# Kernel optimization log

Hardware: AMD Instinct MI355X
Metric: run time of the kernel (lower is better)

## Reference

```python
import jax, jax.numpy as jnp
import numpy as np

N_USERS = 100000
N_ITEMS = 50000
N_NODES = N_USERS + N_ITEMS
N_EDGES = 3000000
EMBED_DIM = 64
N_LAYERS = 3


def setup_inputs() -> dict:
    key = jax.random.key(0)
    k1, k2, k3, k4, k5 = jax.random.split(key, 5)
    user_emb = 0.1 * jax.random.normal(k1, (N_USERS, EMBED_DIM), dtype=jnp.float32)
    item_emb = 0.1 * jax.random.normal(k2, (N_ITEMS, EMBED_DIM), dtype=jnp.float32)
    adj_rows = jax.random.randint(k3, (N_EDGES,), 0, N_NODES, dtype=jnp.int32)
    adj_cols = jax.random.randint(k4, (N_EDGES,), 0, N_NODES, dtype=jnp.int32)
    # mimic symmetric normalization scale (~1/avg_degree) so repeated SpMM stays stable
    avg_degree = N_EDGES / N_NODES
    adj_vals = jax.random.uniform(k5, (N_EDGES,), dtype=jnp.float32) / jnp.float32(avg_degree)
    return {"user_emb": user_emb, "item_emb": item_emb,
            "adj_rows": adj_rows, "adj_cols": adj_cols, "adj_vals": adj_vals}


def _spmm(rows, cols, vals, x):
    # y[r] = sum_{e: rows[e]==r} vals[e] * x[cols[e]]   (COO SpMM)
    msgs = vals[:, None] * x[cols]          # [E, d] gathered messages
    return jax.ops.segment_sum(msgs, rows, num_segments=N_NODES)


def reference(user_emb, item_emb, adj_rows, adj_cols, adj_vals):
    all_emb = jnp.concatenate([user_emb, item_emb], axis=0)  # [N, d]
    acc = all_emb
    cur = all_emb
    for _ in range(N_LAYERS):
        cur = _spmm(adj_rows, adj_cols, adj_vals, cur)
        acc = acc + cur
    final_emb = acc / jnp.float32(N_LAYERS + 1)  # mean over stacked layers
    return final_emb[:N_USERS], final_emb[N_USERS:]
```

## Files before the change

### kernel.cpp

```cpp
#include <hip/hip_runtime.h>
#include <cstddef>
#include <cstdint>

#define N_USERS 100000
#define N_ITEMS 50000
#define N_NODES 150000
#define N_EDGES 3000000

#define NBKT 586
#define BCHUNK 8192
#define ABLK ((N_EDGES + BCHUNK - 1) / BCHUNK)
#define NCLS 16
#define SCHUNK 3

#define VMAX  0.05f
#define QSCALE (16384.0f / VMAX)
#define DEQ    (VMAX / 16384.0f)

typedef unsigned int uint32;
typedef unsigned short ushort16;

__device__ __forceinline__ ushort16 f2b(float f) {
    uint32 b = __float_as_uint(f);
    b += 0x7FFFu + ((b >> 16) & 1u);
    return (ushort16)(b >> 16);
}
__device__ __forceinline__ float b2f(ushort16 h) {
    return __uint_as_float(((uint32)h) << 16);
}

#define CVT_BLOCKS ((N_NODES * 16 + 255) / 256)

__global__ __launch_bounds__(256) void k_cvt_count(const float* __restrict__ user,
                                                   const float* __restrict__ item,
                                                   ushort16* __restrict__ allb,
                                                   const int* __restrict__ rows,
                                                   int* __restrict__ bucket_cnt) {
    if (blockIdx.x < CVT_BLOCKS) {
        int i = blockIdx.x * blockDim.x + threadIdx.x;
        const int total4 = N_NODES * 16;
        if (i >= total4) return;
        const int user4 = N_USERS * 16;
        float4 v = (i < user4) ? ((const float4*)user)[i]
                               : ((const float4*)item)[i - user4];
        ushort4 h;
        h.x = f2b(v.x); h.y = f2b(v.y); h.z = f2b(v.z); h.w = f2b(v.w);
        ((ushort4*)allb)[i] = h;
        return;
    }
    __shared__ int hist[NBKT];
    int t = threadIdx.x;
    for (int j = t; j < NBKT; j += 256) hist[j] = 0;
    __syncthreads();
    int blk = blockIdx.x - CVT_BLOCKS;
    int s0 = blk * BCHUNK;
    int e0 = min(s0 + BCHUNK, N_EDGES);
    for (int i = s0 + t * 4; i < e0; i += 1024) {
        int4 r4 = *(const int4*)(rows + i);
        atomicAdd(&hist[r4.x >> 8], 1); atomicAdd(&hist[r4.y >> 8], 1);
        atomicAdd(&hist[r4.z >> 8], 1); atomicAdd(&hist[r4.w >> 8], 1);
    }
    __syncthreads();
    for (int j = t; j < NBKT; j += 256)
        if (hist[j]) atomicAdd(&bucket_cnt[j], hist[j]);
}

__global__ __launch_bounds__(1024) void k_bucket_scan(const int* __restrict__ bucket_cnt,
                                                      int* __restrict__ bucket_start,
                                                      int* __restrict__ bucket_cursor,
                                                      int* __restrict__ row_start) {
    __shared__ int sh[1024];
    int t = threadIdx.x;
    sh[t] = (t < NBKT) ? bucket_cnt[t] : 0;
    __syncthreads();
    for (int off = 1; off < 1024; off <<= 1) {
        int add = (t >= off) ? sh[t - off] : 0;
        __syncthreads();
        sh[t] += add;
        __syncthreads();
    }
    if (t < NBKT) {
        int st = (t == 0) ? 0 : sh[t - 1];
        bucket_start[t] = st;
        bucket_cursor[t] = st;
    }
    if (t == 0) { bucket_start[NBKT] = N_EDGES; row_start[N_NODES] = N_EDGES; }
}

__global__ __launch_bounds__(256) void k_bucket_scatter(const int* __restrict__ rows,
                                                        const int* __restrict__ cols,
                                                        const float* __restrict__ vals,
                                                        int* __restrict__ bucket_cursor,
                                                        int2* __restrict__ ebuf) {
    __shared__ int  hist[NBKT];
    __shared__ int  lstart[NBKT];
    __shared__ int  curs[NBKT];
    __shared__ int  gbase[NBKT];
    __shared__ int  psum[256];
    __shared__ int2 stage[BCHUNK];
    int t = threadIdx.x;
    for (int j = t; j < NBKT; j += 256) hist[j] = 0;
    __syncthreads();
    int s0 = blockIdx.x * BCHUNK;
    int e0 = min(s0 + BCHUNK, N_EDGES);
    int n = e0 - s0;
    for (int i = s0 + t * 4; i < e0; i += 1024) {
        int4 r4 = *(const int4*)(rows + i);
        atomicAdd(&hist[r4.x >> 8], 1); atomicAdd(&hist[r4.y >> 8], 1);
        atomicAdd(&hist[r4.z >> 8], 1); atomicAdd(&hist[r4.w >> 8], 1);
    }
    __syncthreads();
    int base = t * SCHUNK;
    int v0 = (base < NBKT) ? hist[base] : 0;
    int v1 = (base + 1 < NBKT) ? hist[base + 1] : 0;
    int v2 = (base + 2 < NBKT) ? hist[base + 2] : 0;
    psum[t] = v0 + v1 + v2;
    __syncthreads();
    for (int off = 1; off < 256; off <<= 1) {
        int add = (t >= off) ? psum[t - off] : 0;
        __syncthreads();
        psum[t] += add;
        __syncthreads();
    }
    int run = (t == 0) ? 0 : psum[t - 1];
    if (base < NBKT) {
        lstart[base] = run; curs[base] = run;
        if (v0) gbase[base] = atomicAdd(&bucket_cursor[base], v0);
        run += v0;
    }
    if (base + 1 < NBKT) {
        lstart[base + 1] = run; curs[base + 1] = run;
        if (v1) gbase[base + 1] = atomicAdd(&bucket_cursor[base + 1], v1);
        run += v1;
    }
    if (base + 2 < NBKT) {
        lstart[base + 2] = run; curs[base + 2] = run;
        if (v2) gbase[base + 2] = atomicAdd(&bucket_cursor[base + 2], v2);
        run += v2;
    }
    __syncthreads();
    for (int i = s0 + t * 4; i < e0; i += 1024) {
        int4   r4 = *(const int4*)(rows + i);
        int4   c4 = *(const int4*)(cols + i);
        float4 w4 = *(const float4*)(vals + i);
        int rr, cc, b, pos; float ww;
        rr = r4.x; cc = c4.x; ww = w4.x; b = rr >> 8;
        pos = atomicAdd(&curs[b], 1);
        stage[pos] = make_int2(cc | ((rr & 255) << 18), __float_as_int(ww));
        rr = r4.y; cc = c4.y; ww = w4.y; b = rr >> 8;
        pos = atomicAdd(&curs[b], 1);
        stage[pos] = make_int2(cc | ((rr & 255) << 18), __float_as_int(ww));
        rr = r4.z; cc = c4.z; ww = w4.z; b = rr >> 8;
        pos = atomicAdd(&curs[b], 1);
        stage[pos] = make_int2(cc | ((rr & 255) << 18), __float_as_int(ww));
        rr = r4.w; cc = c4.w; ww = w4.w; b = rr >> 8;
        pos = atomicAdd(&curs[b], 1);
        stage[pos] = make_int2(cc | ((rr & 255) << 18), __float_as_int(ww));
    }
    __syncthreads();
    for (int i = t; i < n; i += 256) {
        int2 ed = stage[i];
        int lo = 0, hi = NBKT - 1;
        while (lo < hi) {
            int mid = (lo + hi + 1) >> 1;
            if (lstart[mid] <= i) lo = mid; else hi = mid - 1;
        }
        int dst = gbase[lo] + (i - lstart[lo]);
        long long q; __builtin_memcpy(&q, &ed, 8);
        __builtin_nontemporal_store(q, (long long*)(ebuf + dst));
    }
}

__global__ __launch_bounds__(256) void k_csr_build(const int2* __restrict__ ebuf,
                                                   const int* __restrict__ bucket_start,
                                                   int* __restrict__ row_start,
                                                   uint32* __restrict__ ecsr) {
    __shared__ int cnt2[256 * NCLS];
    __shared__ int psum[256];
    int b = blockIdx.x, t = threadIdx.x;
    int rbase = b << 8;
    for (int j = t; j < 256 * NCLS; j += 256) cnt2[j] = 0;
    __syncthreads();
    int s = bucket_start[b], e = bucket_start[b + 1];
    for (int i = s + t; i < e; i += 256) {
        int2 ed = ebuf[i];
        int col = ed.x & 0x3FFFF;
        int key = (((ed.x >> 18) & 255) << 4) | (col >> 14);
        atomicAdd(&cnt2[key], 1);
    }
    __syncthreads();
    int base = t * NCLS;
    int vals[NCLS];
    int local = 0;
    #pragma unroll
    for (int j = 0; j < NCLS; ++j) { vals[j] = cnt2[base + j]; local += vals[j]; }
    psum[t] = local;
    __syncthreads();
    for (int off = 1; off < 256; off <<= 1) {
        int add = (t >= off) ? psum[t - off] : 0;
        __syncthreads();
        psum[t] += add;
        __syncthreads();
    }
    int run = (t == 0) ? 0 : psum[t - 1];
    int rr = rbase + t;
    if (rr < N_NODES) row_start[rr] = s + run;
    #pragma unroll
    for (int j = 0; j < NCLS; ++j) { int c = vals[j]; cnt2[base + j] = run; run += c; }
    __syncthreads();
    for (int i = s + t; i < e; i += 256) {
        int2 ed = ebuf[i];
        int col = ed.x & 0x3FFFF;
        int key = (((ed.x >> 18) & 255) << 4) | (col >> 14);
        int pos = atomicAdd(&cnt2[key], 1);
        float w = __int_as_float(ed.y);
        int q = (int)(w * QSCALE + 0.5f);
        q = min(q, 16383);
        ecsr[s + pos] = (uint32)col | ((uint32)q << 18);
    }
}

template <int LAYER>
__global__ __launch_bounds__(256) void k_spmm(const int* __restrict__ row_start,
                                              const uint32* __restrict__ ecsr,
                                              const ushort16* __restrict__ x,
                                              ushort16* __restrict__ yb,
                                              const ushort16* __restrict__ y1b,
                                              const ushort16* __restrict__ y2b,
                                              const float* __restrict__ user,
                                              const float* __restrict__ item,
                                              float* __restrict__ out) {
    int gid = blockIdx.x * blockDim.x + threadIdx.x;
    int r = gid >> 6;
    int lane = threadIdx.x & 63;
    if (r >= N_NODES) return;
    int s = __builtin_amdgcn_readfirstlane(row_start[r]);
    int e = __builtin_amdgcn_readfirstlane(row_start[r + 1]);
    float acc = 0.f;
    int i = s;
    for (; i + 8 <= e; i += 8) {
        uint32 e0 = __builtin_nontemporal_load(ecsr + i);
        uint32 e1 = __builtin_nontemporal_load(ecsr + i + 1);
        uint32 e2 = __builtin_nontemporal_load(ecsr + i + 2);
        uint32 e3 = __builtin_nontemporal_load(ecsr + i + 3);
        uint32 e4 = __builtin_nontemporal_load(ecsr + i + 4);
        uint32 e5 = __builtin_nontemporal_load(ecsr + i + 5);
        uint32 e6 = __builtin_nontemporal_load(ecsr + i + 6);
        uint32 e7 = __builtin_nontemporal_load(ecsr + i + 7);
        float x0 = b2f(x[(size_t)(e0 & 0x3FFFF) * 64 + lane]);
        float x1 = b2f(x[(size_t)(e1 & 0x3FFFF) * 64 + lane]);
        float x2 = b2f(x[(size_t)(e2 & 0x3FFFF) * 64 + lane]);
        float x3 = b2f(x[(size_t)(e3 & 0x3FFFF) * 64 + lane]);
        float x4 = b2f(x[(size_t)(e4 & 0x3FFFF) * 64 + lane]);
        float x5 = b2f(x[(size_t)(e5 & 0x3FFFF) * 64 + lane]);
        float x6 = b2f(x[(size_t)(e6 & 0x3FFFF) * 64 + lane]);
        float x7 = b2f(x[(size_t)(e7 & 0x3FFFF) * 64 + lane]);
        acc += (float)(e0 >> 18) * DEQ * x0; acc += (float)(e1 >> 18) * DEQ * x1;
        acc += (float)(e2 >> 18) * DEQ * x2; acc += (float)(e3 >> 18) * DEQ * x3;
        acc += (float)(e4 >> 18) * DEQ * x4; acc += (float)(e5 >> 18) * DEQ * x5;
        acc += (float)(e6 >> 18) * DEQ * x6; acc += (float)(e7 >> 18) * DEQ * x7;
    }
    for (; i + 4 <= e; i += 4) {
        uint32 e0 = __builtin_nontemporal_load(ecsr + i);
        uint32 e1 = __builtin_nontemporal_load(ecsr + i + 1);
        uint32 e2 = __builtin_nontemporal_load(ecsr + i + 2);
        uint32 e3 = __builtin_nontemporal_load(ecsr + i + 3);
        float x0 = b2f(x[(size_t)(e0 & 0x3FFFF) * 64 + lane]);
        float x1 = b2f(x[(size_t)(e1 & 0x3FFFF) * 64 + lane]);
        float x2 = b2f(x[(size_t)(e2 & 0x3FFFF) * 64 + lane]);
        float x3 = b2f(x[(size_t)(e3 & 0x3FFFF) * 64 + lane]);
        acc += (float)(e0 >> 18) * DEQ * x0; acc += (float)(e1 >> 18) * DEQ * x1;
        acc += (float)(e2 >> 18) * DEQ * x2; acc += (float)(e3 >> 18) * DEQ * x3;
    }
    for (; i < e; ++i) {
        uint32 ed = __builtin_nontemporal_load(ecsr + i);
        acc += (float)(ed >> 18) * DEQ * b2f(x[(size_t)(ed & 0x3FFFF) * 64 + lane]);
    }

    size_t o = (size_t)r * 64 + lane;
    if constexpr (LAYER == 3) {
        float e0v = (r < N_USERS)
            ? __builtin_nontemporal_load(user + o)
            : __builtin_nontemporal_load(item + (o - (size_t)N_USERS * 64));
        ushort16 h1 = __builtin_nontemporal_load((const unsigned short*)y1b + o);
        ushort16 h2 = __builtin_nontemporal_load((const unsigned short*)y2b + o);
        __builtin_nontemporal_store(0.25f * (e0v + b2f(h1) + b2f(h2) + acc), out + o);
    } else {
        __builtin_nontemporal_store(f2b(acc), (unsigned short*)yb + o);
    }
}

__global__ __launch_bounds__(256) void k_init(const float* __restrict__ user,
                                              const float* __restrict__ item,
                                              float* __restrict__ cur,
                                              float* __restrict__ out) {
    int i = blockIdx.x * blockDim.x + threadIdx.x;
    const int total4 = N_NODES * 16;
    if (i >= total4) return;
    const int user4 = N_USERS * 16;
    float4 v = (i < user4) ? ((const float4*)user)[i]
                           : ((const float4*)item)[i - user4];
    ((float4*)cur)[i] = v;
    ((float4*)out)[i] = make_float4(0.25f * v.x, 0.25f * v.y,
                                    0.25f * v.z, 0.25f * v.w);
}

__global__ __launch_bounds__(256) void k_edge_atomic(const int* __restrict__ rows,
                                                     const int* __restrict__ cols,
                                                     const float* __restrict__ vals,
                                                     const float* __restrict__ x,
                                                     float* __restrict__ y) {
    long long gid = (long long)blockIdx.x * blockDim.x + threadIdx.x;
    int e = (int)(gid >> 6);
    int lane = threadIdx.x & 63;
    if (e >= N_EDGES) return;
    int r = rows[e], c = cols[e];
    float v = vals[e];
    atomicAdd(&y[r * 64 + lane], v * x[c * 64 + lane]);
}

__global__ __launch_bounds__(256) void k_accum(const float* __restrict__ y,
                                               float* __restrict__ out) {
    int i = blockIdx.x * blockDim.x + threadIdx.x;
    const int total4 = N_NODES * 16;
    if (i >= total4) return;
    float4 a = ((const float4*)y)[i];
    float4 o = ((float4*)out)[i];
    o.x += 0.25f * a.x; o.y += 0.25f * a.y;
    o.z += 0.25f * a.z; o.w += 0.25f * a.w;
    ((float4*)out)[i] = o;
}

extern "C" void kernel_launch(void* const* d_in, const int* in_sizes, int n_in,
                              void* d_out, int out_size, void* d_ws, size_t ws_size,
                              hipStream_t stream) {
    const float* user = (const float*)d_in[0];
    const float* item = (const float*)d_in[1];
    const int*   rows = (const int*)d_in[2];
    const int*   cols = (const int*)d_in[3];
    const float* vals = (const float*)d_in[4];
    float* out = (float*)d_out;

    const int SPMM_BLOCKS = (N_NODES * 64 + 255) / 256;

    auto align256 = [](size_t x) { return (x + 255) & ~(size_t)255; };
    const size_t sz_embf = align256((size_t)N_NODES * 64 * sizeof(float));
    const size_t sz_embb = align256((size_t)N_NODES * 64 * sizeof(short));
    const size_t sz_ebuf = align256((size_t)N_EDGES * sizeof(int2));
    const size_t sz_ecsr = align256((size_t)N_EDGES * sizeof(uint32));
    const size_t sz_rs   = align256((size_t)(N_NODES + 1) * sizeof(int));
    const size_t sz_bk   = align256((size_t)(NBKT + 1) * sizeof(int));
    const size_t need_csr = 3 * sz_embb + sz_ecsr + sz_rs + 3 * sz_bk;

    char* p = (char*)d_ws;
    if (ws_size >= need_csr) {
        ushort16* allb = (ushort16*)p; p += sz_embb;
        ushort16* y1b  = (ushort16*)p; p += sz_embb;
        ushort16* y2b  = (ushort16*)p; p += sz_embb;
        uint32* ecsr     = (uint32*)p; p += sz_ecsr;
        int*   row_start = (int*)p;   p += sz_rs;
        int*   bucket_cnt    = (int*)p; p += sz_bk;
        int*   bucket_start  = (int*)p; p += sz_bk;
        int*   bucket_cursor = (int*)p; p += sz_bk;
        int2*  ebuf = (int2*)y1b;

        hipMemsetAsync(bucket_cnt, 0, (size_t)NBKT * sizeof(int), stream);
        k_cvt_count<<<CVT_BLOCKS + ABLK, 256, 0, stream>>>(user, item, allb, rows, bucket_cnt);
        k_bucket_scan<<<1, 1024, 0, stream>>>(bucket_cnt, bucket_start, bucket_cursor, row_start);
        k_bucket_scatter<<<ABLK, 256, 0, stream>>>(rows, cols, vals, bucket_cursor, ebuf);
        k_csr_build<<<NBKT, 256, 0, stream>>>(ebuf, bucket_start, row_start, ecsr);

        k_spmm<1><<<SPMM_BLOCKS, 256, 0, stream>>>(row_start, ecsr, allb,
                                                   y1b, nullptr, nullptr, user, item, out);
        k_spmm<2><<<SPMM_BLOCKS, 256, 0, stream>>>(row_start, ecsr, y1b,
                                                   y2b, nullptr, nullptr, user, item, out);
        k_spmm<3><<<SPMM_BLOCKS, 256, 0, stream>>>(row_start, ecsr, y2b,
                                                   nullptr, y1b, y2b, user, item, out);
    } else {
        float* bufA = (float*)p; p += sz_embf;
        float* bufB = (float*)p; p += sz_embf;
        float* in   = bufA;
        float* y    = bufB;
        const long long EA_THREADS = (long long)N_EDGES * 64;
        const int EA_BLOCKS = (int)((EA_THREADS + 255) / 256);

        k_init<<<CVT_BLOCKS, 256, 0, stream>>>(user, item, in, out);
        for (int l = 0; l < 3; ++l) {
            hipMemsetAsync(y, 0, (size_t)N_NODES * 64 * sizeof(float), stream);
            k_edge_atomic<<<EA_BLOCKS, 256, 0, stream>>>(rows, cols, vals, in, y);
            k_accum<<<CVT_BLOCKS, 256, 0, stream>>>(y, out);
            float* t = in; in = y; y = t;
        }
    }
}
```

Measured before the change: 324.3 us.

## Pad CSR rows to multiples of eight and software-pipeline SpMM edge loads

CSR construction now pads every row's edge list to a multiple of eight with zero-weight entries, stores a separate row_end array, and reserves per-bucket slack in the edge array. This lets the SpMM drop its 4-wide and scalar tail loops and use one loop that prefetches the next eight edge words while gathering the current eight. The dequantisation scale is applied once per row instead of once per edge. The final layer reads the bf16 copy of the input embeddings instead of the fp32 originals. The padding adds roughly a sixth more edge reads and redundant gathers of node 0, and the bf16 read slightly reduces the precision of the layer-0 term.

```diff
diff --git a/kernel.cpp b/kernel.cpp
--- a/kernel.cpp
+++ b/kernel.cpp
@@ -12,6 +12,7 @@
 #define ABLK ((N_EDGES + BCHUNK - 1) / BCHUNK)
 #define NCLS 16
 #define SCHUNK 3
+#define PADMAX (256 * 7)
 
 #define VMAX  0.05f
 #define QSCALE (16384.0f / VMAX)
@@ -67,8 +68,7 @@
 
 __global__ __launch_bounds__(1024) void k_bucket_scan(const int* __restrict__ bucket_cnt,
                                                       int* __restrict__ bucket_start,
-                                                      int* __restrict__ bucket_cursor,
-                                                      int* __restrict__ row_start) {
+                                                      int* __restrict__ bucket_cursor) {
     __shared__ int sh[1024];
     int t = threadIdx.x;
     sh[t] = (t < NBKT) ? bucket_cnt[t] : 0;
@@ -84,7 +84,7 @@
         bucket_start[t] = st;
         bucket_cursor[t] = st;
     }
-    if (t == 0) { bucket_start[NBKT] = N_EDGES; row_start[N_NODES] = N_EDGES; }
+    if (t == 0) bucket_start[NBKT] = N_EDGES;
 }
 
 __global__ __launch_bounds__(256) void k_bucket_scatter(const int* __restrict__ rows,
@@ -174,6 +174,7 @@
 __global__ __launch_bounds__(256) void k_csr_build(const int2* __restrict__ ebuf,
                                                    const int* __restrict__ bucket_start,
                                                    int* __restrict__ row_start,
+                                                   int* __restrict__ row_end,
                                                    uint32* __restrict__ ecsr) {
     __shared__ int cnt2[256 * NCLS];
     __shared__ int psum[256];
@@ -182,6 +183,7 @@
     for (int j = t; j < 256 * NCLS; j += 256) cnt2[j] = 0;
     __syncthreads();
     int s = bucket_start[b], e = bucket_start[b + 1];
+    int wbase = s + b * PADMAX;
     for (int i = s + t; i < e; i += 256) {
         int2 ed = ebuf[i];
         int col = ed.x & 0x3FFFF;
@@ -191,10 +193,11 @@
     __syncthreads();
     int base = t * NCLS;
     int vals[NCLS];
-    int local = 0;
+    int cnt_row = 0;
     #pragma unroll
-    for (int j = 0; j < NCLS; ++j) { vals[j] = cnt2[base + j]; local += vals[j]; }
-    psum[t] = local;
+    for (int j = 0; j < NCLS; ++j) { vals[j] = cnt2[base + j]; cnt_row += vals[j]; }
+    int pcnt = (cnt_row + 7) & ~7;
+    psum[t] = pcnt;
     __syncthreads();
     for (int off = 1; off < 256; off <<= 1) {
         int add = (t >= off) ? psum[t - off] : 0;
@@ -202,11 +205,15 @@
         psum[t] += add;
         __syncthreads();
     }
-    int run = (t == 0) ? 0 : psum[t - 1];
+    int run = psum[t] - pcnt;
     int rr = rbase + t;
-    if (rr < N_NODES) row_start[rr] = s + run;
+    if (rr < N_NODES) {
+        row_start[rr] = wbase + run;
+        row_end[rr]   = wbase + run + pcnt;
+    }
+    int rl = run;
     #pragma unroll
-    for (int j = 0; j < NCLS; ++j) { int c = vals[j]; cnt2[base + j] = run; run += c; }
+    for (int j = 0; j < NCLS; ++j) { int c = vals[j]; cnt2[base + j] = rl; rl += c; }
     __syncthreads();
     for (int i = s + t; i < e; i += 256) {
         int2 ed = ebuf[i];
@@ -216,75 +223,73 @@
         float w = __int_as_float(ed.y);
         int q = (int)(w * QSCALE + 0.5f);
         q = min(q, 16383);
-        ecsr[s + pos] = (uint32)col | ((uint32)q << 18);
-    }
+        ecsr[wbase + pos] = (uint32)col | ((uint32)q << 18);
+    }
+    for (int j = cnt_row; j < pcnt; ++j) ecsr[wbase + run + j] = 0;
 }
 
 template <int LAYER>
 __global__ __launch_bounds__(256) void k_spmm(const int* __restrict__ row_start,
+                                              const int* __restrict__ row_end,
                                               const uint32* __restrict__ ecsr,
                                               const ushort16* __restrict__ x,
                                               ushort16* __restrict__ yb,
+                                              const ushort16* __restrict__ e0b,
                                               const ushort16* __restrict__ y1b,
-                                              const ushort16* __restrict__ y2b,
-                                              const float* __restrict__ user,
-                                              const float* __restrict__ item,
                                               float* __restrict__ out) {
     int gid = blockIdx.x * blockDim.x + threadIdx.x;
     int r = gid >> 6;
     int lane = threadIdx.x & 63;
     if (r >= N_NODES) return;
     int s = __builtin_amdgcn_readfirstlane(row_start[r]);
-    int e = __builtin_amdgcn_readfirstlane(row_start[r + 1]);
+    int e = __builtin_amdgcn_readfirstlane(row_end[r]);
     float acc = 0.f;
-    int i = s;
-    for (; i + 8 <= e; i += 8) {
-        uint32 e0 = __builtin_nontemporal_load(ecsr + i);
-        uint32 e1 = __builtin_nontemporal_load(ecsr + i + 1);
-        uint32 e2 = __builtin_nontemporal_load(ecsr + i + 2);
-        uint32 e3 = __builtin_nontemporal_load(ecsr + i + 3);
-        uint32 e4 = __builtin_nontemporal_load(ecsr + i + 4);
-        uint32 e5 = __builtin_nontemporal_load(ecsr + i + 5);
-        uint32 e6 = __builtin_nontemporal_load(ecsr + i + 6);
-        uint32 e7 = __builtin_nontemporal_load(ecsr + i + 7);
-        float x0 = b2f(x[(size_t)(e0 & 0x3FFFF) * 64 + lane]);
-        float x1 = b2f(x[(size_t)(e1 & 0x3FFFF) * 64 + lane]);
-        float x2 = b2f(x[(size_t)(e2 & 0x3FFFF) * 64 + lane]);
-        float x3 = b2f(x[(size_t)(e3 & 0x3FFFF) * 64 + lane]);
-        float x4 = b2f(x[(size_t)(e4 & 0x3FFFF) * 64 + lane]);
-        float x5 = b2f(x[(size_t)(e5 & 0x3FFFF) * 64 + lane]);
-        float x6 = b2f(x[(size_t)(e6 & 0x3FFFF) * 64 + lane]);
-        float x7 = b2f(x[(size_t)(e7 & 0x3FFFF) * 64 + lane]);
-        acc += (float)(e0 >> 18) * DEQ * x0; acc += (float)(e1 >> 18) * DEQ * x1;
-        acc += (float)(e2 >> 18) * DEQ * x2; acc += (float)(e3 >> 18) * DEQ * x3;
-        acc += (float)(e4 >> 18) * DEQ * x4; acc += (float)(e5 >> 18) * DEQ * x5;
-        acc += (float)(e6 >> 18) * DEQ * x6; acc += (float)(e7 >> 18) * DEQ * x7;
-    }
-    for (; i + 4 <= e; i += 4) {
-        uint32 e0 = __builtin_nontemporal_load(ecsr + i);
-        uint32 e1 = __builtin_nontemporal_load(ecsr + i + 1);
-        uint32 e2 = __builtin_nontemporal_load(ecsr + i + 2);
-        uint32 e3 = __builtin_nontemporal_load(ecsr + i + 3);
-        float x0 = b2f(x[(size_t)(e0 & 0x3FFFF) * 64 + lane]);
-        float x1 = b2f(x[(size_t)(e1 & 0x3FFFF) * 64 + lane]);
-        float x2 = b2f(x[(size_t)(e2 & 0x3FFFF) * 64 + lane]);
-        float x3 = b2f(x[(size_t)(e3 & 0x3FFFF) * 64 + lane]);
-        acc += (float)(e0 >> 18) * DEQ * x0; acc += (float)(e1 >> 18) * DEQ * x1;
-        acc += (float)(e2 >> 18) * DEQ * x2; acc += (float)(e3 >> 18) * DEQ * x3;
-    }
-    for (; i < e; ++i) {
-        uint32 ed = __builtin_nontemporal_load(ecsr + i);
-        acc += (float)(ed >> 18) * DEQ * b2f(x[(size_t)(ed & 0x3FFFF) * 64 + lane]);
+    if (e > s) {
+        uint32 c0 = __builtin_nontemporal_load(ecsr + s);
+        uint32 c1 = __builtin_nontemporal_load(ecsr + s + 1);
+        uint32 c2 = __builtin_nontemporal_load(ecsr + s + 2);
+        uint32 c3 = __builtin_nontemporal_load(ecsr + s + 3);
+        uint32 c4 = __builtin_nontemporal_load(ecsr + s + 4);
+        uint32 c5 = __builtin_nontemporal_load(ecsr + s + 5);
+        uint32 c6 = __builtin_nontemporal_load(ecsr + s + 6);
+        uint32 c7 = __builtin_nontemporal_load(ecsr + s + 7);
+        for (int i = s + 8; i < e; i += 8) {
+            uint32 n0 = __builtin_nontemporal_load(ecsr + i);
+            uint32 n1 = __builtin_nontemporal_load(ecsr + i + 1);
+            uint32 n2 = __builtin_nontemporal_load(ecsr + i + 2);
+            uint32 n3 = __builtin_nontemporal_load(ecsr + i + 3);
+            uint32 n4 = __builtin_nontemporal_load(ecsr + i + 4);
+            uint32 n5 = __builtin_nontemporal_load(ecsr + i + 5);
+            uint32 n6 = __builtin_nontemporal_load(ecsr + i + 6);
+            uint32 n7 = __builtin_nontemporal_load(ecsr + i + 7);
+            acc += (float)(c0 >> 18) * b2f(x[(size_t)(c0 & 0x3FFFF) * 64 + lane]);
+            acc += (float)(c1 >> 18) * b2f(x[(size_t)(c1 & 0x3FFFF) * 64 + lane]);
+            acc += (float)(c2 >> 18) * b2f(x[(size_t)(c2 & 0x3FFFF) * 64 + lane]);
+            acc += (float)(c3 >> 18) * b2f(x[(size_t)(c3 & 0x3FFFF) * 64 + lane]);
+            acc += (float)(c4 >> 18) * b2f(x[(size_t)(c4 & 0x3FFFF) * 64 + lane]);
+            acc += (float)(c5 >> 18) * b2f(x[(size_t)(c5 & 0x3FFFF) * 64 + lane]);
+            acc += (float)(c6 >> 18) * b2f(x[(size_t)(c6 & 0x3FFFF) * 64 + lane]);
+            acc += (float)(c7 >> 18) * b2f(x[(size_t)(c7 & 0x3FFFF) * 64 + lane]);
+            c0 = n0; c1 = n1; c2 = n2; c3 = n3;
+            c4 = n4; c5 = n5; c6 = n6; c7 = n7;
+        }
+        acc += (float)(c0 >> 18) * b2f(x[(size_t)(c0 & 0x3FFFF) * 64 + lane]);
+        acc += (float)(c1 >> 18) * b2f(x[(size_t)(c1 & 0x3FFFF) * 64 + lane]);
+        acc += (float)(c2 >> 18) * b2f(x[(size_t)(c2 & 0x3FFFF) * 64 + lane]);
+        acc += (float)(c3 >> 18) * b2f(x[(size_t)(c3 & 0x3FFFF) * 64 + lane]);
+        acc += (float)(c4 >> 18) * b2f(x[(size_t)(c4 & 0x3FFFF) * 64 + lane]);
+        acc += (float)(c5 >> 18) * b2f(x[(size_t)(c5 & 0x3FFFF) * 64 + lane]);
+        acc += (float)(c6 >> 18) * b2f(x[(size_t)(c6 & 0x3FFFF) * 64 + lane]);
+        acc += (float)(c7 >> 18) * b2f(x[(size_t)(c7 & 0x3FFFF) * 64 + lane]);
+        acc *= DEQ;
     }
 
     size_t o = (size_t)r * 64 + lane;
     if constexpr (LAYER == 3) {
-        float e0v = (r < N_USERS)
-            ? __builtin_nontemporal_load(user + o)
-            : __builtin_nontemporal_load(item + (o - (size_t)N_USERS * 64));
+        ushort16 h0 = __builtin_nontemporal_load((const unsigned short*)e0b + o);
         ushort16 h1 = __builtin_nontemporal_load((const unsigned short*)y1b + o);
-        ushort16 h2 = __builtin_nontemporal_load((const unsigned short*)y2b + o);
-        __builtin_nontemporal_store(0.25f * (e0v + b2f(h1) + b2f(h2) + acc), out + o);
+        ushort16 h2 = __builtin_nontemporal_load((const unsigned short*)x + o);
+        __builtin_nontemporal_store(0.25f * (b2f(h0) + b2f(h1) + b2f(h2) + acc), out + o);
     } else {
         __builtin_nontemporal_store(f2b(acc), (unsigned short*)yb + o);
     }
@@ -346,11 +351,11 @@
     auto align256 = [](size_t x) { return (x + 255) & ~(size_t)255; };
     const size_t sz_embf = align256((size_t)N_NODES * 64 * sizeof(float));
     const size_t sz_embb = align256((size_t)N_NODES * 64 * sizeof(short));
-    const size_t sz_ebuf = align256((size_t)N_EDGES * sizeof(int2));
-    const size_t sz_ecsr = align256((size_t)N_EDGES * sizeof(uint32));
+    const size_t n_ecsr  = (size_t)N_EDGES + (size_t)NBKT * PADMAX;
+    const size_t sz_ecsr = align256(n_ecsr * sizeof(uint32));
     const size_t sz_rs   = align256((size_t)(N_NODES + 1) * sizeof(int));
     const size_t sz_bk   = align256((size_t)(NBKT + 1) * sizeof(int));
-    const size_t need_csr = 3 * sz_embb + sz_ecsr + sz_rs + 3 * sz_bk;
+    const size_t need_csr = 3 * sz_embb + sz_ecsr + 2 * sz_rs + 3 * sz_bk;
 
     char* p = (char*)d_ws;
     if (ws_size >= need_csr) {
@@ -359,6 +364,7 @@
         ushort16* y2b  = (ushort16*)p; p += sz_embb;
         uint32* ecsr     = (uint32*)p; p += sz_ecsr;
         int*   row_start = (int*)p;   p += sz_rs;
+        int*   row_end   = (int*)p;   p += sz_rs;
         int*   bucket_cnt    = (int*)p; p += sz_bk;
         int*   bucket_start  = (int*)p; p += sz_bk;
         int*   bucket_cursor = (int*)p; p += sz_bk;
@@ -366,16 +372,16 @@
 
         hipMemsetAsync(bucket_cnt, 0, (size_t)NBKT * sizeof(int), stream);
         k_cvt_count<<<CVT_BLOCKS + ABLK, 256, 0, stream>>>(user, item, allb, rows, bucket_cnt);
-        k_bucket_scan<<<1, 1024, 0, stream>>>(bucket_cnt, bucket_start, bucket_cursor, row_start);
+        k_bucket_scan<<<1, 1024, 0, stream>>>(bucket_cnt, bucket_start, bucket_cursor);
         k_bucket_scatter<<<ABLK, 256, 0, stream>>>(rows, cols, vals, bucket_cursor, ebuf);
-        k_csr_build<<<NBKT, 256, 0, stream>>>(ebuf, bucket_start, row_start, ecsr);
-
-        k_spmm<1><<<SPMM_BLOCKS, 256, 0, stream>>>(row_start, ecsr, allb,
-                                                   y1b, nullptr, nullptr, user, item, out);
-        k_spmm<2><<<SPMM_BLOCKS, 256, 0, stream>>>(row_start, ecsr, y1b,
-                                                   y2b, nullptr, nullptr, user, item, out);
-        k_spmm<3><<<SPMM_BLOCKS, 256, 0, stream>>>(row_start, ecsr, y2b,
-                                                   nullptr, y1b, y2b, user, item, out);
+        k_csr_build<<<NBKT, 256, 0, stream>>>(ebuf, bucket_start, row_start, row_end, ecsr);
+
+        k_spmm<1><<<SPMM_BLOCKS, 256, 0, stream>>>(row_start, row_end, ecsr, allb,
+                                                   y1b, nullptr, nullptr, out);
+        k_spmm<2><<<SPMM_BLOCKS, 256, 0, stream>>>(row_start, row_end, ecsr, y1b,
+                                                   y2b, nullptr, nullptr, out);
+        k_spmm<3><<<SPMM_BLOCKS, 256, 0, stream>>>(row_start, row_end, ecsr, y2b,
+                                                   nullptr, allb, y1b, out);
     } else {
         float* bufA = (float*)p; p += sz_embf;
         float* bufB = (float*)p; p += sz_embf;
```

Measured after the change: 309.5 us. 1.05x faster.
